# Kernel tuning notes

Measured on AMD Instinct MI355X. Metric: run time of the kernel, lower is better.

## Reference

```python
import jax, jax.numpy as jnp
import numpy as np

LAMBDA = 150.0


def setup_inputs() -> dict:
    key = jax.random.key(0)
    k1, k2 = jax.random.split(key)
    gru_outputs = jax.random.normal(k1, (8192, 4096), dtype=jnp.float32)
    target = jax.random.normal(k2, (8192, 4096), dtype=jnp.float32)
    return {"gru_outputs": gru_outputs, "target": target}


def reference(gru_outputs, target):
    # L1Loss with default 'mean' reduction
    l1_loss = jnp.mean(jnp.abs(gru_outputs - target))
    # smooth_loss: for each element hr_t of gru_outputs[:6].flatten(),
    # MyLoss.forward returns |hr_t - mean(hr_outs)|; summed then divided by T
    # => mean(|x - mean(x)|), computed in one fused pass instead of a python loop.
    x = gru_outputs[:6].reshape(-1)
    smooth = jnp.mean(jnp.abs(x - jnp.mean(x)))
    return l1_loss + LAMBDA * smooth
```

## Files before the change

### kernel.cpp

```cpp
#include <hip/hip_runtime.h>


#define N_TOTAL  (8192 * 4096)
#define N_SMOOTH (6 * 4096)
#define LAMBDA_F 150.0f

constexpr int BLOCKS  = 2048;
constexpr int THREADS = 256;
constexpr int N4           = N_TOTAL / 4;
constexpr int F4_PER_BLOCK = N4 / BLOCKS;
constexpr int ITERS        = F4_PER_BLOCK / THREADS;
constexpr int NT_BLOCKS = 768;

typedef float vf4 __attribute__((ext_vector_type(4)));

template <int NT>
__device__ __forceinline__ float block_reduce_bcast(float v) {
    __shared__ float ws[NT / 64 + 1];
    __syncthreads();
    #pragma unroll
    for (int off = 32; off > 0; off >>= 1) v += __shfl_down(v, off, 64);
    const int lane = threadIdx.x & 63;
    const int wid  = threadIdx.x >> 6;
    if (lane == 0) ws[wid] = v;
    __syncthreads();
    if (threadIdx.x == 0) {
        float s = 0.0f;
        #pragma unroll
        for (int w = 0; w < NT / 64; ++w) s += ws[w];
        ws[NT / 64] = s;
    }
    __syncthreads();
    return ws[NT / 64];
}

__device__ __forceinline__ float abs4(vf4 va, vf4 vb) {
    return fabsf(va.x - vb.x) + fabsf(va.y - vb.y) +
           fabsf(va.z - vb.z) + fabsf(va.w - vb.w);
}

template <bool NTLOAD>
__device__ __forceinline__ vf4 ld4(const vf4* p) {
    if constexpr (NTLOAD) return __builtin_nontemporal_load(p);
    else                  return *p;
}

template <bool NTLOAD>
__device__ __forceinline__ float l1_chunk(const vf4* __restrict__ a,
                                          const vf4* __restrict__ b) {
    const int base = blockIdx.x * F4_PER_BLOCK + threadIdx.x;
    float s0 = 0.0f, s1 = 0.0f, s2 = 0.0f, s3 = 0.0f;
    #pragma unroll
    for (int g = 0; g < ITERS / 4; ++g) {
        const int i0 = base + (g * 4 + 0) * THREADS;
        const int i1 = base + (g * 4 + 1) * THREADS;
        const int i2 = base + (g * 4 + 2) * THREADS;
        const int i3 = base + (g * 4 + 3) * THREADS;
        vf4 a0 = ld4<NTLOAD>(a + i0); vf4 a1 = ld4<NTLOAD>(a + i1);
        vf4 a2 = ld4<NTLOAD>(a + i2); vf4 a3 = ld4<NTLOAD>(a + i3);
        vf4 b0 = ld4<NTLOAD>(b + i0); vf4 b1 = ld4<NTLOAD>(b + i1);
        vf4 b2 = ld4<NTLOAD>(b + i2); vf4 b3 = ld4<NTLOAD>(b + i3);
        s0 += abs4(a0, b0);
        s1 += abs4(a1, b1);
        s2 += abs4(a2, b2);
        s3 += abs4(a3, b3);
    }
    return (s0 + s1) + (s2 + s3);
}

__global__ __launch_bounds__(THREADS) void l1_partial_kernel(
    const vf4* __restrict__ a, const vf4* __restrict__ b,
    float* __restrict__ partial) {
    if (blockIdx.x < BLOCKS) {
        float s = (blockIdx.x < NT_BLOCKS) ? l1_chunk<true>(a, b)
                                           : l1_chunk<false>(a, b);
        float bs = block_reduce_bcast<THREADS>(s);
        if (threadIdx.x == 0) partial[blockIdx.x] = bs;
    } else {
        constexpr int NS4 = N_SMOOTH / 4;
        float xs = 0.0f;
        for (int i = threadIdx.x; i < NS4; i += THREADS) {
            vf4 v = a[i];
            xs += (v.x + v.y) + (v.z + v.w);
        }
        float x_mean = block_reduce_bcast<THREADS>(xs) / (float)N_SMOOTH;
        float ds = 0.0f;
        for (int i = threadIdx.x; i < NS4; i += THREADS) {
            vf4 v = a[i];
            ds += fabsf(v.x - x_mean) + fabsf(v.y - x_mean) +
                  fabsf(v.z - x_mean) + fabsf(v.w - x_mean);
        }
        float dev_sum = block_reduce_bcast<THREADS>(ds);
        if (threadIdx.x == 0) partial[BLOCKS] = dev_sum;
    }
}

__global__ __launch_bounds__(THREADS) void finalize_kernel(
    const float* __restrict__ partial, float* __restrict__ out) {
    const vf4* p4 = (const vf4*)partial;
    float s = 0.0f;
    #pragma unroll
    for (int i = threadIdx.x; i < BLOCKS / 4; i += THREADS) {
        vf4 v = p4[i];
        s += (v.x + v.y) + (v.z + v.w);
    }
    float l1_sum = block_reduce_bcast<THREADS>(s);
    if (threadIdx.x == 0) {
        float dev_sum = partial[BLOCKS];
        out[0] = l1_sum / (float)N_TOTAL + LAMBDA_F * (dev_sum / (float)N_SMOOTH);
    }
}

extern "C" void kernel_launch(void* const* d_in, const int* in_sizes, int n_in,
                              void* d_out, int out_size, void* d_ws, size_t ws_size,
                              hipStream_t stream) {
    const float* gru = (const float*)d_in[0];
    const float* tgt = (const float*)d_in[1];
    float* out     = (float*)d_out;
    float* partial = (float*)d_ws;

    l1_partial_kernel<<<BLOCKS + 1, THREADS, 0, stream>>>(
        (const vf4*)gru, (const vf4*)tgt, partial);
    finalize_kernel<<<1, THREADS, 0, stream>>>(partial, out);
}
```

Before: 48.29 us.

## Fuse finalize into main kernel via last-block ticket and drop nontemporal loads

Replaces the separate finalize kernel with a last-block-done pattern. Each block publishes its partial with an atomic store, takes a ticket with atomicAdd, and the final block sums all partials and writes the output. The ticket is reset by a hipMemsetAsync before the launch. It also removes the split between nontemporal and regular loads so every block uses plain loads. This saves a second kernel launch at the cost of a memset and a fence/atomic per block, and it changes the cache behaviour of the streaming loads.

```diff
diff --git a/kernel.cpp b/kernel.cpp
--- a/kernel.cpp
+++ b/kernel.cpp
@@ -10,7 +10,6 @@
 constexpr int N4           = N_TOTAL / 4;
 constexpr int F4_PER_BLOCK = N4 / BLOCKS;
 constexpr int ITERS        = F4_PER_BLOCK / THREADS;
-constexpr int NT_BLOCKS = 768;
 
 typedef float vf4 __attribute__((ext_vector_type(4)));
 
@@ -39,13 +38,6 @@
            fabsf(va.z - vb.z) + fabsf(va.w - vb.w);
 }
 
-template <bool NTLOAD>
-__device__ __forceinline__ vf4 ld4(const vf4* p) {
-    if constexpr (NTLOAD) return __builtin_nontemporal_load(p);
-    else                  return *p;
-}
-
-template <bool NTLOAD>
 __device__ __forceinline__ float l1_chunk(const vf4* __restrict__ a,
                                           const vf4* __restrict__ b) {
     const int base = blockIdx.x * F4_PER_BLOCK + threadIdx.x;
@@ -56,10 +48,8 @@
         const int i1 = base + (g * 4 + 1) * THREADS;
         const int i2 = base + (g * 4 + 2) * THREADS;
         const int i3 = base + (g * 4 + 3) * THREADS;
-        vf4 a0 = ld4<NTLOAD>(a + i0); vf4 a1 = ld4<NTLOAD>(a + i1);
-        vf4 a2 = ld4<NTLOAD>(a + i2); vf4 a3 = ld4<NTLOAD>(a + i3);
-        vf4 b0 = ld4<NTLOAD>(b + i0); vf4 b1 = ld4<NTLOAD>(b + i1);
-        vf4 b2 = ld4<NTLOAD>(b + i2); vf4 b3 = ld4<NTLOAD>(b + i3);
+        vf4 a0 = a[i0]; vf4 a1 = a[i1]; vf4 a2 = a[i2]; vf4 a3 = a[i3];
+        vf4 b0 = b[i0]; vf4 b1 = b[i1]; vf4 b2 = b[i2]; vf4 b3 = b[i3];
         s0 += abs4(a0, b0);
         s1 += abs4(a1, b1);
         s2 += abs4(a2, b2);
@@ -68,14 +58,18 @@
     return (s0 + s1) + (s2 + s3);
 }
 
-__global__ __launch_bounds__(THREADS) void l1_partial_kernel(
+__global__ __launch_bounds__(THREADS) void rhythm_loss_kernel(
     const vf4* __restrict__ a, const vf4* __restrict__ b,
-    float* __restrict__ partial) {
-    if (blockIdx.x < BLOCKS) {
-        float s = (blockIdx.x < NT_BLOCKS) ? l1_chunk<true>(a, b)
-                                           : l1_chunk<false>(a, b);
-        float bs = block_reduce_bcast<THREADS>(s);
-        if (threadIdx.x == 0) partial[blockIdx.x] = bs;
+    float* __restrict__ partial, unsigned* __restrict__ ticket,
+    float* __restrict__ out) {
+    const int bid = blockIdx.x;
+
+    if (bid < BLOCKS) {
+        float bs = block_reduce_bcast<THREADS>(l1_chunk(a, b));
+        if (threadIdx.x == 0) {
+            __hip_atomic_store(&partial[bid], bs, __ATOMIC_RELAXED,
+                               __HIP_MEMORY_SCOPE_AGENT);
+        }
     } else {
         constexpr int NS4 = N_SMOOTH / 4;
         float xs = 0.0f;
@@ -91,23 +85,31 @@
                   fabsf(v.z - x_mean) + fabsf(v.w - x_mean);
         }
         float dev_sum = block_reduce_bcast<THREADS>(ds);
-        if (threadIdx.x == 0) partial[BLOCKS] = dev_sum;
+        if (threadIdx.x == 0) {
+            __hip_atomic_store(&partial[BLOCKS], dev_sum, __ATOMIC_RELAXED,
+                               __HIP_MEMORY_SCOPE_AGENT);
+        }
     }
-}
 
-__global__ __launch_bounds__(THREADS) void finalize_kernel(
-    const float* __restrict__ partial, float* __restrict__ out) {
-    const vf4* p4 = (const vf4*)partial;
-    float s = 0.0f;
-    #pragma unroll
-    for (int i = threadIdx.x; i < BLOCKS / 4; i += THREADS) {
-        vf4 v = p4[i];
-        s += (v.x + v.y) + (v.z + v.w);
+    __shared__ unsigned last;
+    if (threadIdx.x == 0) {
+        __threadfence();
+        unsigned old = atomicAdd(ticket, 1u);
+        last = (old == (unsigned)BLOCKS) ? 1u : 0u;
     }
-    float l1_sum = block_reduce_bcast<THREADS>(s);
-    if (threadIdx.x == 0) {
-        float dev_sum = partial[BLOCKS];
-        out[0] = l1_sum / (float)N_TOTAL + LAMBDA_F * (dev_sum / (float)N_SMOOTH);
+    __syncthreads();
+    if (last) {
+        float s = 0.0f;
+        #pragma unroll
+        for (int i = threadIdx.x; i < BLOCKS; i += THREADS)
+            s += __hip_atomic_load(&partial[i], __ATOMIC_RELAXED,
+                                   __HIP_MEMORY_SCOPE_AGENT);
+        float l1_sum = block_reduce_bcast<THREADS>(s);
+        if (threadIdx.x == 0) {
+            float dev_sum = __hip_atomic_load(&partial[BLOCKS], __ATOMIC_RELAXED,
+                                              __HIP_MEMORY_SCOPE_AGENT);
+            out[0] = l1_sum / (float)N_TOTAL + LAMBDA_F * (dev_sum / (float)N_SMOOTH);
+        }
     }
 }
 
@@ -118,8 +120,9 @@
     const float* tgt = (const float*)d_in[1];
     float* out     = (float*)d_out;
     float* partial = (float*)d_ws;
+    unsigned* ticket = (unsigned*)((char*)d_ws + 8448);
 
-    l1_partial_kernel<<<BLOCKS + 1, THREADS, 0, stream>>>(
-        (const vf4*)gru, (const vf4*)tgt, partial);
-    finalize_kernel<<<1, THREADS, 0, stream>>>(partial, out);
+    hipMemsetAsync(ticket, 0, sizeof(unsigned), stream);
+    rhythm_loss_kernel<<<BLOCKS + 1, THREADS, 0, stream>>>(
+        (const vf4*)gru, (const vf4*)tgt, partial, ticket, out);
 }
```

Result: slower. 117.2 us (+142.7%).
